# Performance work log

Hardware: AMD Instinct MI355X
Metric: run time of the kernel (lower is better)

## Reference

```python
import jax, jax.numpy as jnp
import numpy as np

B, NPER, K = 32, 256, 32
N, E = B * NPER, B * NPER * 32
H, NF, NG, L = 128, 128, 50, 6
CUTOFF = 10.0
LOG2 = 0.6931471805599453


def _ssp(x):
    # ShiftedSoftplus: softplus(x) - log(2)
    return jax.nn.softplus(x) - LOG2


def setup_inputs() -> dict:
    key = jax.random.key(0)
    ks = jax.random.split(key, 16)
    rng = np.random.default_rng(0)

    pos = jnp.asarray(rng.uniform(0.0, 5.0, size=(N, 3)).astype(np.float32))
    z = jnp.asarray(rng.integers(1, 100, size=(N,)).astype(np.int32))
    batch = jnp.asarray((np.arange(N) // NPER).astype(np.int32))
    # K neighbors per atom, within the same graph, no self-loops; dst sorted
    dst = np.repeat(np.arange(N), K)
    off = rng.integers(1, NPER, size=N * K)
    src = (dst % NPER + off) % NPER + (dst // NPER) * NPER
    edge_index = jnp.asarray(np.stack([src, dst]).astype(np.int32))
    domain_ids = jnp.asarray(rng.integers(0, 5, size=(B,)).astype(np.int32))

    def dense(k, i, o):
        return jax.random.normal(k, (i, o), jnp.float32) / np.sqrt(i)

    def stackw(k, i, o):
        return jax.random.normal(k, (L, i, o), jnp.float32) / np.sqrt(i)

    return {
        'pos': pos, 'z': z, 'batch': batch, 'edge_index': edge_index,
        'domain_ids': domain_ids,
        'embedding': jax.random.normal(ks[0], (100, H), jnp.float32),
        'mlp_w1': stackw(ks[1], NG, NF), 'mlp_b1': jnp.zeros((L, NF), jnp.float32),
        'mlp_w2': stackw(ks[2], NF, NF), 'mlp_b2': jnp.zeros((L, NF), jnp.float32),
        'cf_lin1_w': stackw(ks[3], H, NF),
        'cf_lin2_w': stackw(ks[4], NF, H), 'cf_lin2_b': jnp.zeros((L, H), jnp.float32),
        'int_lin_w': stackw(ks[5], H, H), 'int_lin_b': jnp.zeros((L, H), jnp.float32),
        'out_w1': dense(ks[6], H, H // 2), 'out_b1': jnp.zeros((H // 2,), jnp.float32),
        'out_w2': dense(ks[7], H // 2, 1), 'out_b2': jnp.zeros((1,), jnp.float32),
        'dom_emb': jax.random.normal(ks[8], (5, 64), jnp.float32),
        'film_w1': dense(ks[9], 64, 128), 'film_b1': jnp.zeros((128,), jnp.float32),
        'film_w2': dense(ks[10], 128, 128), 'film_b2': jnp.zeros((128,), jnp.float32),
        'gamma_w': dense(ks[11], 128, H), 'gamma_b': jnp.zeros((H,), jnp.float32),
        'beta_w': dense(ks[12], 128, H), 'beta_b': jnp.zeros((H,), jnp.float32),
    }


def reference(pos, z, batch, edge_index, domain_ids, embedding,
              mlp_w1, mlp_b1, mlp_w2, mlp_b2, cf_lin1_w, cf_lin2_w, cf_lin2_b,
              int_lin_w, int_lin_b, out_w1, out_b1, out_w2, out_b2,
              dom_emb, film_w1, film_b1, film_w2, film_b2,
              gamma_w, gamma_b, beta_w, beta_b):
    n_atoms = pos.shape[0]
    n_graphs = domain_ids.shape[0]
    src, dst = edge_index[0], edge_index[1]

    # edge distances, gaussian smearing, cosine cutoff (computed once)
    d = jnp.sqrt(jnp.sum((pos[src] - pos[dst]) ** 2, axis=-1))          # [E]
    offsets = jnp.linspace(0.0, CUTOFF, NG).astype(pos.dtype)
    coeff = -0.5 / (CUTOFF / (NG - 1)) ** 2
    edge_attr = jnp.exp(coeff * (d[:, None] - offsets) ** 2)            # [E,NG]
    C = 0.5 * (jnp.cos(d * (np.pi / CUTOFF)) + 1.0)                     # [E]

    h = embedding[z]                                                    # [N,H]
    for l in range(L):
        # filter network on gaussian basis, modulated by cosine cutoff
        W = (_ssp(edge_attr @ mlp_w1[l] + mlp_b1[l]) @ mlp_w2[l] + mlp_b2[l]) * C[:, None]  # [E,NF]
        x = h @ cf_lin1_w[l]                                            # [N,NF]
        msg = x[src] * W                                                # [E,NF]
        agg = jax.ops.segment_sum(msg, dst, num_segments=n_atoms)       # [N,NF]
        x = agg @ cf_lin2_w[l] + cf_lin2_b[l]                           # [N,H]
        h = h + _ssp(x) @ int_lin_w[l] + int_lin_b[l]                   # residual

    atom_e = _ssp(h @ out_w1 + out_b1) @ out_w2 + out_b2                # [N,1]
    e_graph = jax.ops.segment_sum(atom_e, batch, num_segments=n_graphs) # [B,1]

    # FiLM domain bias (features are zeros, so gamma path contributes 0 - faithful)
    de = dom_emb[domain_ids]                                            # [B,64]
    film = jax.nn.relu(de @ film_w1 + film_b1) @ film_w2 + film_b2      # [B,128]
    gamma = film @ gamma_w + gamma_b                                    # [B,H]
    beta = film @ beta_w + beta_b                                       # [B,H]
    dummy = jnp.zeros((n_graphs, H), pos.dtype)
    bias = jnp.sum(gamma * dummy + beta, axis=-1)                       # [B]

    # faithful broadcast [B,1]+[B] -> [B,B], then sum(dim=1) as in original
    energy = jnp.sum(e_graph + bias[None, :], axis=1)                   # [B]

    forces = jnp.zeros((n_atoms, 3), energy.dtype)
    stress = jnp.zeros((n_graphs, 3, 3), energy.dtype)
    features = jnp.zeros((n_atoms, H), energy.dtype)
    return energy, forces, stress, features
```

## Files before the change

kernel.cpp:

```cpp
#include <hip/hip_runtime.h>
#include <math.h>

using uint = unsigned int;
typedef _Float16 h2    __attribute__((ext_vector_type(2)));
typedef _Float16 f16x8 __attribute__((ext_vector_type(8)));
typedef float    f32x4 __attribute__((ext_vector_type(4)));

#define N_ATOMS 8192
#define NEDGE   262144
#define KNBR    32
#define NGAUSS  50
#define NLAYER  6
#define NB      32
#define GTAB    1024
#define DMAX    8.6603f
#define FCUT    10.0f
#define MB      1048576

#define LSTRIDE 76
#define S_WT    0
#define S_AS    9728
#define S_TS    10944
#define GEMM_SMEM 12160

#define T_W1    0
#define T_W2    4096
#define T_RBF   12288
#define T_HID   13312
#define TAB_SMEM 15360

#define OW1P_OFF 147456
#define M1_OFF   151552
#define M2_OFF   176128
#define WPACK_N  225280

__device__ __forceinline__ float ssp(float x) {
    return fmaxf(x, 0.0f) + log1pf(expf(-fabsf(x))) - 0.69314718055994531f;
}
__device__ __forceinline__ uint pack2(float a, float b) {
    union { h2 h; uint u; } x;
    h2 v; v.x = (_Float16)a; v.y = (_Float16)b; x.h = v; return x.u;
}
__device__ __forceinline__ h2 u2h(uint u) {
    union { uint u; h2 h; } x; x.u = u; return x.h;
}
__device__ __forceinline__ uint h2u(h2 h) {
    union { h2 h; uint u; } x; x.h = h; return x.u;
}
__device__ __forceinline__ float fdot2f(h2 a, h2 b, float c) {
#if __has_builtin(__builtin_amdgcn_fdot2)
    return __builtin_amdgcn_fdot2(a, b, c, false);
#else
    return fmaf((float)a.y, (float)b.y, fmaf((float)a.x, (float)b.x, c));
#endif
}

__device__ __forceinline__ void stage_cp(uint* sm, const uint* __restrict__ src,
                                         int n16, int tid) {
    for (int i = tid; i < n16; i += 256) {
        uint4 v = ((const uint4*)src)[i];
        *(uint4*)&sm[(i >> 4) * LSTRIDE + (i & 15) * 4] = v;
    }
}

template<int NCT>
__device__ __forceinline__ void run_gemm(const uint* sm, int as_off, int lane,
                                         int nb, f32x4* acc) {
    int m = lane & 15, q = lane >> 4;
    #pragma unroll
    for (int ks = 0; ks < 4; ++ks) {
        f16x8 a = *(const f16x8*)&sm[as_off + m * LSTRIDE + q * 4 + ks * 16];
        #pragma unroll
        for (int ct = 0; ct < NCT; ++ct) {
            f16x8 b = *(const f16x8*)&sm[S_WT + (nb + ct * 16 + m) * LSTRIDE + q * 4 + ks * 16];
            acc[ct] = __builtin_amdgcn_mfma_f32_16x16x32_f16(a, b, acc[ct], 0, 0, 0);
        }
    }
}

struct SArgs {
    const float *pos; const int *z; const int *ei; const int *dom;
    const float *emb;
    const float *cf1; const float *cf2w; const float *intw; const float *ow1;
    const float *mw1; const float *mw2;
    const float *dome; const float *fw1; const float *fb1;
    const float *fw2; const float *fb2; const float *bw; const float *bb;
    uint2 *epack; float *h; uint *xA;
    float *gbias; uint *wpack; float *out; int out_size;
};

__global__ void __launch_bounds__(256) k_setup(SArgs a) {
    __shared__ __align__(16) uint sm[S_AS + 1216];
    const int tid = threadIdx.x, bid = blockIdx.x;
    const int gidx = bid * 256 + tid, gsz = 512 * 256;
    const int lane = tid & 63, w = tid >> 6;
    const int m = lane & 15, q = lane >> 4;
    const int rowbase = bid * 16;

    for (int i = gidx; i < a.out_size; i += gsz) a.out[i] = 0.0f;

    for (int idx = gidx; idx < WPACK_N; idx += gsz) {
        if (idx < OW1P_OFF) {
            int mat = idx >> 13, e = idx & 8191;
            int kp = e >> 7, cc = e & 127;
            const float* src = (mat < 6) ? (a.cf1 + mat * 16384)
                            : (mat < 12) ? (a.cf2w + (mat - 6) * 16384)
                                         : (a.intw + (mat - 12) * 16384);
            a.wpack[mat * 8192 + cc * 64 + kp] =
                pack2(src[2 * kp * 128 + cc], src[(2 * kp + 1) * 128 + cc]);
        } else if (idx < M1_OFF) {
            int e = idx - OW1P_OFF;
            int kp = e >> 6, cc = e & 63;
            a.wpack[OW1P_OFF + cc * 64 + kp] =
                pack2(a.ow1[2 * kp * 64 + cc], a.ow1[(2 * kp + 1) * 64 + cc]);
        } else if (idx < M2_OFF) {
            int e = idx - M1_OFF;
            int l = e >> 12, r = e & 4095;
            int kp = r >> 7, cc = r & 127;
            int g0 = 2 * kp;
            float va = (g0 < NGAUSS)     ? a.mw1[l*NGAUSS*128 + g0*128 + cc]     : 0.f;
            float vb = (g0 + 1 < NGAUSS) ? a.mw1[l*NGAUSS*128 + (g0+1)*128 + cc] : 0.f;
            a.wpack[idx] = pack2(va, vb);
        } else {
            int e = idx - M2_OFF;
            int l = e >> 13, r = e & 8191;
            int kp = r >> 7, cc = r & 127;
            a.wpack[idx] = pack2(a.mw2[l*16384 + 2*kp*128 + cc],
                                 a.mw2[l*16384 + (2*kp+1)*128 + cc]);
        }
    }

    const float invdelta = (float)(GTAB - 1) / DMAX;
    #pragma unroll
    for (int t = 0; t < 2; ++t) {
        int e = rowbase * KNBR + t * 256 + tid;
        int s = a.ei[e], d = a.ei[NEDGE + e];
        float dx = a.pos[3*s] - a.pos[3*d];
        float dy = a.pos[3*s+1] - a.pos[3*d+1];
        float dz = a.pos[3*s+2] - a.pos[3*d+2];
        float dist = sqrtf(dx*dx + dy*dy + dz*dz);
        float u = dist * invdelta;
        int i0 = (int)u; i0 = (i0 < GTAB - 2) ? i0 : (GTAB - 2);
        float t2 = u - (float)i0;
        uint tb = pack2(t2, 0.0f) & 0xffffu;
        uint2 ep; ep.x = (uint)s; ep.y = (tb << 16) | (uint)i0;
        a.epack[e] = ep;
    }

    for (int i = tid; i < 1024; i += 256) {
        int r = i >> 6, f2 = i & 63;
        int zz = a.z[rowbase + r];
        float2 v = *(const float2*)&a.emb[zz * 128 + f2 * 2];
        *(float2*)&a.h[(rowbase + r) * 128 + f2 * 2] = v;
        sm[S_AS + r * LSTRIDE + f2] = pack2(v.x, v.y);
    }
    for (int i = tid; i < 2048; i += 256) {
        int m4 = i >> 7, cc = i & 127;
        float v[8];
        #pragma unroll
        for (int j = 0; j < 8; ++j) v[j] = a.cf1[(8 * m4 + j) * 128 + cc];
        uint4 pk; pk.x = pack2(v[0], v[1]); pk.y = pack2(v[2], v[3]);
        pk.z = pack2(v[4], v[5]); pk.w = pack2(v[6], v[7]);
        *(uint4*)&sm[cc * LSTRIDE + m4 * 4] = pk;
    }
    __syncthreads();
    {
        f32x4 acc[2] = {{0,0,0,0},{0,0,0,0}};
        run_gemm<2>(sm, S_AS, lane, w * 32, acc);
        #pragma unroll
        for (int ct = 0; ct < 2; ++ct) {
            int n = w * 32 + ct * 16 + m;
            #pragma unroll
            for (int i = 0; i < 4; ++i) {
                float v = acc[ct][i];
                float u = __shfl_xor(v, 1, 64);
                if (!(lane & 1))
                    a.xA[(rowbase + q * 4 + i) * 64 + (n >> 1)] = pack2(v, u);
            }
        }
    }
    __syncthreads();
    if (bid >= 32 && bid < 64) {
        int g = bid - 32;
        float* fs = (float*)sm;
        if (tid < 64) fs[tid] = a.dome[a.dom[g] * 64 + tid];
        __syncthreads();
        if (tid < 128) {
            float acc = a.fb1[tid];
            for (int i = 0; i < 64; ++i) acc = fmaf(fs[i], a.fw1[i*128 + tid], acc);
            fs[64 + tid] = fmaxf(acc, 0.0f);
        }
        __syncthreads();
        if (tid < 128) {
            float acc = a.fb2[tid];
            for (int i = 0; i < 128; ++i) acc = fmaf(fs[64+i], a.fw2[i*128 + tid], acc);
            fs[192 + tid] = acc;
        }
        __syncthreads();
        if (tid < 128) {
            float acc = a.bb[tid];
            for (int i = 0; i < 128; ++i) acc = fmaf(fs[192+i], a.bw[i*128 + tid], acc);
            #pragma unroll
            for (int off = 32; off > 0; off >>= 1) acc += __shfl_down(acc, off, 64);
            if ((tid & 63) == 0) fs[320 + (tid >> 6)] = acc;
        }
        __syncthreads();
        if (tid == 0) a.gbias[g] = fs[320] + fs[321];
    }
}

__global__ void __launch_bounds__(256) k_table(
    const uint* __restrict__ wpack, const float* __restrict__ mb1,
    const float* __restrict__ mb2, uint* __restrict__ tab2) {
    __shared__ __align__(16) uint sm[TAB_SMEM];
    const int tid = threadIdx.x;
    const int l = blockIdx.x >> 5;
    const int base = (blockIdx.x & 31) * 32;
    { const uint4* s4 = (const uint4*)(wpack + M1_OFF + l*4096);
      uint4* d4 = (uint4*)&sm[T_W1];
      for (int i = tid; i < 1024; i += 256) d4[i] = s4[i]; }
    { const uint4* s4 = (const uint4*)(wpack + M2_OFF + l*8192);
      uint4* d4 = (uint4*)&sm[T_W2];
      for (int i = tid; i < 2048; i += 256) d4[i] = s4[i]; }
    const float delta = DMAX / (float)(GTAB - 1);
    const float gstep = FCUT / (float)(NGAUSS - 1);
    const float coeff = -0.5f / (gstep * gstep);
    for (int i = tid; i < 1024; i += 256) {
        int r = i >> 5, kp = i & 31;
        float dv = (float)(base + r) * delta;
        int g0 = 2 * kp;
        float v0 = 0.f, v1 = 0.f;
        if (g0 < NGAUSS)     { float t = dv - (float)g0 * gstep;     v0 = expf(coeff*t*t); }
        if (g0 + 1 < NGAUSS) { float t = dv - (float)(g0+1) * gstep; v1 = expf(coeff*t*t); }
        sm[T_RBF + i] = pack2(v0, v1);
    }
    __syncthreads();
    int tx = tid & 31, ty = tid >> 5, c0 = tx * 4, tr0 = ty * 4;
    float acc[4][4];
    #pragma unroll
    for (int i = 0; i < 4; ++i) { acc[i][0]=0.f; acc[i][1]=0.f; acc[i][2]=0.f; acc[i][3]=0.f; }
    #pragma unroll
    for (int oct = 0; oct < 8; ++oct) {
        int kp0 = oct * 4;
        uint4 w_[4];
        #pragma unroll
        for (int p = 0; p < 4; ++p) w_[p] = *(const uint4*)&sm[T_W1 + (kp0+p)*128 + c0];
        #pragma unroll
        for (int i = 0; i < 4; ++i) {
            uint4 av = *(const uint4*)&sm[T_RBF + (tr0+i)*32 + kp0];
            uint aa[4] = {av.x, av.y, av.z, av.w};
            #pragma unroll
            for (int p = 0; p < 4; ++p) {
                h2 ap = u2h(aa[p]);
                acc[i][0] = fdot2f(ap, u2h(w_[p].x), acc[i][0]);
                acc[i][1] = fdot2f(ap, u2h(w_[p].y), acc[i][1]);
                acc[i][2] = fdot2f(ap, u2h(w_[p].z), acc[i][2]);
                acc[i][3] = fdot2f(ap, u2h(w_[p].w), acc[i][3]);
            }
        }
    }
    float4 b1v = *(const float4*)&mb1[l*128 + c0];
    #pragma unroll
    for (int i = 0; i < 4; ++i) {
        uint2 o;
        o.x = pack2(ssp(acc[i][0] + b1v.x), ssp(acc[i][1] + b1v.y));
        o.y = pack2(ssp(acc[i][2] + b1v.z), ssp(acc[i][3] + b1v.w));
        *(uint2*)&sm[T_HID + (tr0+i)*64 + (c0 >> 1)] = o;
    }
    __syncthreads();
    float acc2[4][4];
    #pragma unroll
    for (int i = 0; i < 4; ++i) { acc2[i][0]=0.f; acc2[i][1]=0.f; acc2[i][2]=0.f; acc2[i][3]=0.f; }
    #pragma unroll 4
    for (int oct = 0; oct < 16; ++oct) {
        int kp0 = oct * 4;
        uint4 w_[4];
        #pragma unroll
        for (int p = 0; p < 4; ++p) w_[p] = *(const uint4*)&sm[T_W2 + (kp0+p)*128 + c0];
        #pragma unroll
        for (int i = 0; i < 4; ++i) {
            uint4 av = *(const uint4*)&sm[T_HID + (tr0+i)*64 + kp0];
            uint aa[4] = {av.x, av.y, av.z, av.w};
            #pragma unroll
            for (int p = 0; p < 4; ++p) {
                h2 ap = u2h(aa[p]);
                acc2[i][0] = fdot2f(ap, u2h(w_[p].x), acc2[i][0]);
                acc2[i][1] = fdot2f(ap, u2h(w_[p].y), acc2[i][1]);
                acc2[i][2] = fdot2f(ap, u2h(w_[p].z), acc2[i][2]);
                acc2[i][3] = fdot2f(ap, u2h(w_[p].w), acc2[i][3]);
            }
        }
    }
    float4 b2v = *(const float4*)&mb2[l*128 + c0];
    #pragma unroll
    for (int i = 0; i < 4; ++i) {
        int row = base + tr0 + i;
        float dv = (float)row * delta;
        float Cd = 0.5f * (cosf(dv * 0.3141592653589793f) + 1.0f);
        uint2 o;
        o.x = pack2((acc2[i][0] + b2v.x)*Cd, (acc2[i][1] + b2v.y)*Cd);
        o.y = pack2((acc2[i][2] + b2v.z)*Cd, (acc2[i][3] + b2v.w)*Cd);
        *(uint2*)&tab2[(l*GTAB + row)*128 + tx*4] = o;
        if (row > 0)
            *(uint2*)&tab2[(l*GTAB + row - 1)*128 + tx*4 + 2] = o;
    }
}

template<bool LAST>
__global__ void __launch_bounds__(256) k_layer(
    float* __restrict__ h, const uint* __restrict__ xin, uint* __restrict__ xout,
    const uint* __restrict__ tab2l, const uint2* __restrict__ epack,
    const uint* __restrict__ w2p, const uint* __restrict__ w3p,
    const uint* __restrict__ w1np,
    const float* __restrict__ b2, const float* __restrict__ b3,
    const float* __restrict__ ob1, const float* __restrict__ ow2,
    const float* __restrict__ ob2, const float* __restrict__ gbias,
    float* __restrict__ out) {
    __shared__ __align__(16) uint sm[GEMM_SMEM];
    const int tid = threadIdx.x, bid = blockIdx.x;
    const int lane = tid & 63, w = tid >> 6;
    const int m = lane & 15, q = lane >> 4;
    const int rowbase = bid * 16;

    stage_cp(sm, w2p, 2048, tid);
    {
        const int side = lane >> 5, l5 = lane & 31;
        #pragma unroll
        for (int p = 0; p < 4; ++p) {
            int al = p * 4 + w;
            uint2 ep = epack[(rowbase + al) * KNBR + l5];
            h2 a0; a0.x = (_Float16)0; a0.y = (_Float16)0;
            h2 a1 = a0;
            #pragma unroll 4
            for (int k = 0; k < 16; ++k) {
                int e = 2 * k + side;
                uint s = __shfl(ep.x, e, 64);
                uint y = __shfl(ep.y, e, 64);
                int i0 = (int)(y & 0xffffu);
                uint th = y >> 16;
                h2 t2 = u2h(th | (th << 16));
                uint4 tv = *(const uint4*)&tab2l[i0 * 128 + l5 * 4];
                uint2 xv = *(const uint2*)&xin[s * 64 + l5 * 2];
                h2 w0 = u2h(tv.x) + t2 * (u2h(tv.z) - u2h(tv.x));
                h2 w1 = u2h(tv.y) + t2 * (u2h(tv.w) - u2h(tv.y));
                a0 = a0 + u2h(xv.x) * w0;
                a1 = a1 + u2h(xv.y) * w1;
            }
            uint u0 = h2u(a0), u1 = h2u(a1);
            uint p0 = __shfl_xor(u0, 32, 64), p1 = __shfl_xor(u1, 32, 64);
            if (side == 0) {
                h2 r0 = u2h(u0) + u2h(p0), r1 = u2h(u1) + u2h(p1);
                uint2 o; o.x = h2u(r0); o.y = h2u(r1);
                *(uint2*)&sm[S_AS + al * LSTRIDE + l5 * 2] = o;
            }
        }
    }
    __syncthreads();
    {
        f32x4 acc[2] = {{0,0,0,0},{0,0,0,0}};
        run_gemm<2>(sm, S_AS, lane, w * 32, acc);
        #pragma unroll
        for (int ct = 0; ct < 2; ++ct) {
            int n = w * 32 + ct * 16 + m;
            float bv = b2[n];
            #pragma unroll
            for (int i = 0; i < 4; ++i) {
                float v = ssp(acc[ct][i] + bv);
                float u = __shfl_xor(v, 1, 64);
                if (!(lane & 1))
                    sm[S_TS + (q * 4 + i) * LSTRIDE + (n >> 1)] = pack2(v, u);
            }
        }
    }
    __syncthreads();
    stage_cp(sm, w3p, 2048, tid);
    __syncthreads();
    {
        f32x4 acc[2] = {{0,0,0,0},{0,0,0,0}};
        run_gemm<2>(sm, S_TS, lane, w * 32, acc);
        #pragma unroll
        for (int ct = 0; ct < 2; ++ct) {
            int n = w * 32 + ct * 16 + m;
            float bv = b3[n];
            #pragma unroll
            for (int i = 0; i < 4; ++i) {
                int r = rowbase + q * 4 + i;
                float hv = h[r * 128 + n] + acc[ct][i] + bv;
                h[r * 128 + n] = hv;
                float u = __shfl_xor(hv, 1, 64);
                if (!(lane & 1))
                    sm[S_AS + (q * 4 + i) * LSTRIDE + (n >> 1)] = pack2(hv, u);
            }
        }
    }
    __syncthreads();
    if (!LAST) {
        stage_cp(sm, w1np, 2048, tid);
        __syncthreads();
        f32x4 acc[2] = {{0,0,0,0},{0,0,0,0}};
        run_gemm<2>(sm, S_AS, lane, w * 32, acc);
        #pragma unroll
        for (int ct = 0; ct < 2; ++ct) {
            int n = w * 32 + ct * 16 + m;
            #pragma unroll
            for (int i = 0; i < 4; ++i) {
                float v = acc[ct][i];
                float u = __shfl_xor(v, 1, 64);
                if (!(lane & 1))
                    xout[(rowbase + q * 4 + i) * 64 + (n >> 1)] = pack2(v, u);
            }
        }
    } else {
        stage_cp(sm, w1np, 1024, tid);
        __syncthreads();
        f32x4 acc[1] = {{0,0,0,0}};
        run_gemm<1>(sm, S_AS, lane, w * 16, acc);
        int n = w * 16 + m;
        float b1v = ob1[n], w2v = ow2[n];
        float part = 0.f;
        #pragma unroll
        for (int i = 0; i < 4; ++i) part += ssp(acc[0][i] + b1v) * w2v;
        #pragma unroll
        for (int mm = 1; mm < 64; mm <<= 1) part += __shfl_xor(part, mm, 64);
        float* fs = (float*)&sm[S_TS];
        if (lane == 0) fs[w] = part;
        __syncthreads();
        if (tid == 0) {
            float bsum = fs[0] + fs[1] + fs[2] + fs[3] + 16.0f * ob2[0];
            float add = 32.0f * bsum;
            if ((bid & 15) == 0) {
                float sb = 0.f;
                for (int j = 0; j < NB; ++j) sb += gbias[j];
                add += sb;
            }
            atomicAdd(&out[bid >> 4], add);
        }
    }
}

extern "C" void kernel_launch(void* const* d_in, const int* in_sizes, int n_in,
                              void* d_out, int out_size, void* d_ws, size_t ws_size,
                              hipStream_t stream) {
    SArgs a;
    a.pos  = (const float*)d_in[0];
    a.z    = (const int*)d_in[1];
    a.ei   = (const int*)d_in[3];
    a.dom  = (const int*)d_in[4];
    a.emb  = (const float*)d_in[5];
    a.mw1  = (const float*)d_in[6];
    const float* mb1 = (const float*)d_in[7];
    a.mw2  = (const float*)d_in[8];
    const float* mb2 = (const float*)d_in[9];
    a.cf1  = (const float*)d_in[10];
    a.cf2w = (const float*)d_in[11];
    const float* cf2b = (const float*)d_in[12];
    a.intw = (const float*)d_in[13];
    const float* intb = (const float*)d_in[14];
    a.ow1  = (const float*)d_in[15];
    const float* ob1  = (const float*)d_in[16];
    const float* ow2  = (const float*)d_in[17];
    const float* ob2  = (const float*)d_in[18];
    a.dome = (const float*)d_in[19];
    a.fw1  = (const float*)d_in[20];
    a.fb1  = (const float*)d_in[21];
    a.fw2  = (const float*)d_in[22];
    a.fb2  = (const float*)d_in[23];
    a.bw   = (const float*)d_in[26];
    a.bb   = (const float*)d_in[27];

    char* ws = (char*)d_ws;
    a.epack   = (uint2*)(ws + 0);
    uint* tab2= (uint*)(ws + 2*MB);
    a.h       = (float*)(ws + 5*MB);
    a.xA      = (uint*)(ws + 9*MB);
    uint* xB  = (uint*)(ws + 11*MB);
    a.gbias   = (float*)(ws + 15*MB);
    a.wpack   = (uint*)(ws + 15*MB + 4096);
    a.out = (float*)d_out;
    a.out_size = out_size;

    k_setup<<<512, 256, 0, stream>>>(a);
    k_table<<<192, 256, 0, stream>>>(a.wpack, mb1, mb2, tab2);

    const uint* xr = a.xA;
    uint* xw = xB;
    for (int l = 0; l < NLAYER; ++l) {
        const uint* w2p = a.wpack + (6 + l) * 8192;
        const uint* w3p = a.wpack + (12 + l) * 8192;
        if (l < NLAYER - 1) {
            k_layer<false><<<512, 256, 0, stream>>>(
                a.h, xr, xw, tab2 + l*GTAB*128, a.epack, w2p, w3p,
                a.wpack + (l + 1) * 8192,
                cf2b + l*128, intb + l*128, ob1, ow2, ob2, a.gbias, a.out);
        } else {
            k_layer<true><<<512, 256, 0, stream>>>(
                a.h, xr, xw, tab2 + l*GTAB*128, a.epack, w2p, w3p,
                a.wpack + OW1P_OFF,
                cf2b + l*128, intb + l*128, ob1, ow2, ob2, a.gbias, a.out);
        }
        const uint* tmp = xr; xr = xw; xw = (uint*)tmp;
    }
}
```

Before: 268.9 us.

## Double-buffer layer weights in swizzled LDS and prefetch h residual

Replaces the padded-stride LDS layout with an XOR-swizzled layout and splits weight storage into two buffers. The next GEMM's weights can then be staged while the current GEMM runs, which removes the separate stage-then-sync steps before the second and third GEMMs. The residual h values are loaded into registers at kernel start instead of being re-read at the epilogue. LDS use grows from about 48KB to 72KB per block, which may lower occupancy.

```diff
diff --git a/kernel.cpp b/kernel.cpp
--- a/kernel.cpp
+++ b/kernel.cpp
@@ -20,8 +20,12 @@
 #define LSTRIDE 76
 #define S_WT    0
 #define S_AS    9728
-#define S_TS    10944
-#define GEMM_SMEM 12160
+
+#define WA_OFF  0
+#define WB_OFF  8192
+#define AS_OFF  16384
+#define TS_OFF  17408
+#define LAY_N   18432
 
 #define T_W1    0
 #define T_W2    4096
@@ -55,11 +59,35 @@
 #endif
 }
 
-__device__ __forceinline__ void stage_cp(uint* sm, const uint* __restrict__ src,
+__device__ __forceinline__ int swz(int row, int quad) {
+    return row * 64 + ((quad ^ (row & 15)) << 2);
+}
+__device__ __forceinline__ int swzc(int row, int c) {
+    return row * 64 + (((c >> 2) ^ (row & 15)) << 2) + (c & 3);
+}
+
+__device__ __forceinline__ void stage_sw(uint* dst, const uint* __restrict__ src,
                                          int n16, int tid) {
     for (int i = tid; i < n16; i += 256) {
         uint4 v = ((const uint4*)src)[i];
-        *(uint4*)&sm[(i >> 4) * LSTRIDE + (i & 15) * 4] = v;
+        *(uint4*)&dst[swz(i >> 4, i & 15)] = v;
+    }
+}
+
+template<int NCT>
+__device__ __forceinline__ void run_gemm_sw(const uint* smA, const uint* smW,
+                                            int lane, int nb, f32x4* acc) {
+    int m = lane & 15, q = lane >> 4;
+    #pragma unroll
+    for (int ks = 0; ks < 4; ++ks) {
+        int cq = q + ks * 4;
+        f16x8 a = *(const f16x8*)&smA[swz(m, cq)];
+        #pragma unroll
+        for (int ct = 0; ct < NCT; ++ct) {
+            int n = nb + ct * 16 + m;
+            f16x8 b = *(const f16x8*)&smW[swz(n, cq)];
+            acc[ct] = __builtin_amdgcn_mfma_f32_16x16x32_f16(a, b, acc[ct], 0, 0, 0);
+        }
     }
 }
 
@@ -316,13 +344,20 @@
     const float* __restrict__ ob1, const float* __restrict__ ow2,
     const float* __restrict__ ob2, const float* __restrict__ gbias,
     float* __restrict__ out) {
-    __shared__ __align__(16) uint sm[GEMM_SMEM];
+    __shared__ __align__(16) uint sm[LAY_N];
     const int tid = threadIdx.x, bid = blockIdx.x;
     const int lane = tid & 63, w = tid >> 6;
     const int m = lane & 15, q = lane >> 4;
     const int rowbase = bid * 16;
 
-    stage_cp(sm, w2p, 2048, tid);
+    float hr[2][4];
+    #pragma unroll
+    for (int ct = 0; ct < 2; ++ct)
+        #pragma unroll
+        for (int i = 0; i < 4; ++i)
+            hr[ct][i] = h[(rowbase + q * 4 + i) * 128 + w * 32 + ct * 16 + m];
+
+    stage_sw(&sm[WA_OFF], w2p, 2048, tid);
     {
         const int side = lane >> 5, l5 = lane & 31;
         #pragma unroll
@@ -351,14 +386,15 @@
             if (side == 0) {
                 h2 r0 = u2h(u0) + u2h(p0), r1 = u2h(u1) + u2h(p1);
                 uint2 o; o.x = h2u(r0); o.y = h2u(r1);
-                *(uint2*)&sm[S_AS + al * LSTRIDE + l5 * 2] = o;
-            }
-        }
-    }
-    __syncthreads();
+                *(uint2*)&sm[AS_OFF + swzc(al, l5 * 2)] = o;
+            }
+        }
+    }
+    __syncthreads();
+    stage_sw(&sm[WB_OFF], w3p, 2048, tid);
     {
         f32x4 acc[2] = {{0,0,0,0},{0,0,0,0}};
-        run_gemm<2>(sm, S_AS, lane, w * 32, acc);
+        run_gemm_sw<2>(&sm[AS_OFF], &sm[WA_OFF], lane, w * 32, acc);
         #pragma unroll
         for (int ct = 0; ct < 2; ++ct) {
             int n = w * 32 + ct * 16 + m;
@@ -368,16 +404,15 @@
                 float v = ssp(acc[ct][i] + bv);
                 float u = __shfl_xor(v, 1, 64);
                 if (!(lane & 1))
-                    sm[S_TS + (q * 4 + i) * LSTRIDE + (n >> 1)] = pack2(v, u);
-            }
-        }
-    }
-    __syncthreads();
-    stage_cp(sm, w3p, 2048, tid);
-    __syncthreads();
+                    sm[TS_OFF + swzc(q * 4 + i, n >> 1)] = pack2(v, u);
+            }
+        }
+    }
+    __syncthreads();
+    stage_sw(&sm[WA_OFF], w1np, LAST ? 1024 : 2048, tid);
     {
         f32x4 acc[2] = {{0,0,0,0},{0,0,0,0}};
-        run_gemm<2>(sm, S_TS, lane, w * 32, acc);
+        run_gemm_sw<2>(&sm[TS_OFF], &sm[WB_OFF], lane, w * 32, acc);
         #pragma unroll
         for (int ct = 0; ct < 2; ++ct) {
             int n = w * 32 + ct * 16 + m;
@@ -385,20 +420,18 @@
             #pragma unroll
             for (int i = 0; i < 4; ++i) {
                 int r = rowbase + q * 4 + i;
-                float hv = h[r * 128 + n] + acc[ct][i] + bv;
+                float hv = hr[ct][i] + acc[ct][i] + bv;
                 h[r * 128 + n] = hv;
                 float u = __shfl_xor(hv, 1, 64);
                 if (!(lane & 1))
-                    sm[S_AS + (q * 4 + i) * LSTRIDE + (n >> 1)] = pack2(hv, u);
+                    sm[AS_OFF + swzc(q * 4 + i, n >> 1)] = pack2(hv, u);
             }
         }
     }
     __syncthreads();
     if (!LAST) {
-        stage_cp(sm, w1np, 2048, tid);
-        __syncthreads();
         f32x4 acc[2] = {{0,0,0,0},{0,0,0,0}};
-        run_gemm<2>(sm, S_AS, lane, w * 32, acc);
+        run_gemm_sw<2>(&sm[AS_OFF], &sm[WA_OFF], lane, w * 32, acc);
         #pragma unroll
         for (int ct = 0; ct < 2; ++ct) {
             int n = w * 32 + ct * 16 + m;
@@ -411,10 +444,8 @@
             }
         }
     } else {
-        stage_cp(sm, w1np, 1024, tid);
-        __syncthreads();
         f32x4 acc[1] = {{0,0,0,0}};
-        run_gemm<1>(sm, S_AS, lane, w * 16, acc);
+        run_gemm_sw<1>(&sm[AS_OFF], &sm[WA_OFF], lane, w * 16, acc);
         int n = w * 16 + m;
         float b1v = ob1[n], w2v = ow2[n];
         float part = 0.f;
@@ -422,7 +453,7 @@
         for (int i = 0; i < 4; ++i) part += ssp(acc[0][i] + b1v) * w2v;
         #pragma unroll
         for (int mm = 1; mm < 64; mm <<= 1) part += __shfl_xor(part, mm, 64);
-        float* fs = (float*)&sm[S_TS];
+        float* fs = (float*)&sm[TS_OFF];
         if (lane == 0) fs[w] = part;
         __syncthreads();
         if (tid == 0) {
```

New measurement: 267.0 us. No clear change (-0.7%).
